# Kernel optimization log

Measured on AMD Instinct MI355X. Metric: run time of the kernel, lower is better.

Reference implementation:

```python
import jax, jax.numpy as jnp
import numpy as np
from jax import lax

V, E, H, T = 50000, 100, 230, 70
BIG, N = 128, 4096
NR, PV, PD = 53, 123, 5
IN = E + 2 * PD  # GRU input size = embedding_dim + 10


def setup_inputs():
    key = jax.random.key(0)
    ks = jax.random.split(key, 18)
    rng = np.random.default_rng(0)
    sizes = 1 + rng.multinomial(N - BIG, np.ones(BIG) / BIG)  # ragged, nonempty bags
    total_shape = jnp.asarray(np.concatenate([[0], np.cumsum(sizes)]).astype(np.int32))
    nrm = lambda k, s, sc=0.05: jax.random.normal(k, s, dtype=jnp.float32) * sc
    return {
        'sentence': jax.random.randint(ks[0], (N, T), 0, V),
        'pos1': jax.random.randint(ks[1], (N, T), 0, PV),
        'pos2': jax.random.randint(ks[2], (N, T), 0, PV),
        'total_shape': total_shape,
        'y_batch': jax.random.uniform(ks[3], (BIG, NR), dtype=jnp.float32),
        'word_emb': nrm(ks[4], (V, E), 0.1),
        'pos1_emb': nrm(ks[5], (PV, PD), 0.1),
        'pos2_emb': nrm(ks[6], (PV, PD), 0.1),
        'w_ih_f': nrm(ks[7], (3 * H, IN)),
        'w_hh_f': nrm(ks[8], (3 * H, H)),
        'b_ih_f': nrm(ks[9], (3 * H,)),
        'b_hh_f': nrm(ks[10], (3 * H,)),
        'w_ih_b': nrm(ks[11], (3 * H, IN)),
        'w_hh_b': nrm(ks[12], (3 * H, H)),
        'b_ih_b': nrm(ks[13], (3 * H,)),
        'b_hh_b': nrm(ks[14], (3 * H,)),
        'attention_w': nrm(ks[15], (H, 1), 0.1),
        'sen_a': nrm(ks[16], (H,), 0.1),
        'sen_r': nrm(ks[17], (H, 1), 0.1),
        'relation_embedding': nrm(jax.random.fold_in(key, 99), (NR, H), 0.1),
        'sen_d': nrm(jax.random.fold_in(key, 98), (NR,), 0.1),
    }


def _gru(x_proj, w_hh, b_hh, reverse):
    # x_proj: [T, N, 3H] precomputed input projections (PyTorch GRU gate order r,z,n)
    def step(h, xp):
        gh = h @ w_hh.T + b_hh
        r = jax.nn.sigmoid(xp[:, :H] + gh[:, :H])
        z = jax.nn.sigmoid(xp[:, H:2 * H] + gh[:, H:2 * H])
        n = jnp.tanh(xp[:, 2 * H:] + r * gh[:, 2 * H:])
        h = (1.0 - z) * n + z * h
        return h, h
    h0 = jnp.zeros((x_proj.shape[1], H), x_proj.dtype)
    _, hs = lax.scan(step, h0, x_proj, reverse=reverse)
    return hs  # [T, N, H], aligned with input time order


def reference(sentence, pos1, pos2, total_shape, y_batch, word_emb, pos1_emb, pos2_emb,
              w_ih_f, w_hh_f, b_ih_f, b_hh_f, w_ih_b, w_hh_b, b_ih_b, b_hh_b,
              attention_w, sen_a, sen_r, relation_embedding, sen_d):
    x = jnp.concatenate([word_emb[sentence], pos1_emb[pos1], pos2_emb[pos2]], axis=-1)  # [N,T,IN]
    xt = x.transpose(1, 0, 2)  # [T,N,IN]
    hf = _gru(jnp.einsum('tni,gi->tng', xt, w_ih_f) + b_ih_f, w_hh_f, b_hh_f, False)
    hb = _gru(jnp.einsum('tni,gi->tng', xt, w_ih_b) + b_ih_b, w_hh_b, b_hh_b, True)
    tup = (hf + hb).transpose(1, 0, 2)  # [N,T,H] fwd+bwd states summed, as in source
    scores = jnp.einsum('nth,h->nt', jnp.tanh(tup), attention_w[:, 0])
    alpha = jax.nn.softmax(scores, axis=-1)  # word attention over T=70
    attention_r = jnp.einsum('nt,nth->nh', alpha, tup)
    sen_repre = jnp.tanh(attention_r)  # [N,H]
    # ragged per-bag attention via segment ops (replaces Python loop over bags)
    seg = jnp.searchsorted(total_shape, jnp.arange(N), side='right') - 1  # bag id per sentence
    e = jnp.einsum('nh,h->n', sen_repre * sen_a, sen_r[:, 0])
    m = jax.ops.segment_max(e, seg, num_segments=BIG)
    ex = jnp.exp(e - m[seg])
    denom = jax.ops.segment_sum(ex, seg, num_segments=BIG)
    bag_alpha = ex / denom[seg]
    sen_s = jax.ops.segment_sum(bag_alpha[:, None] * sen_repre, seg, num_segments=BIG)  # [BIG,H]
    logits = sen_s @ relation_embedding.T + sen_d  # [BIG,NR]
    prob = jax.nn.softmax(logits, axis=-1)
    pred = jnp.argmax(prob, axis=-1)
    # BCEWithLogits, mean over 53 classes per bag, summed over bags
    bce = y_batch * jax.nn.softplus(-logits) + (1.0 - y_batch) * jax.nn.softplus(logits)
    total_loss = jnp.sum(jnp.mean(bce, axis=-1))
    acc = (pred == jnp.argmax(y_batch, axis=-1)).astype(jnp.float32)  # [BIG]
    return total_loss, acc, prob
```

## Files before the change

### kernel.cpp

```cpp
#include <hip/hip_runtime.h>
#include <hip/hip_bf16.h>
#include <math.h>

#define NSENT 4096
#define TT 70
#define HH 230
#define BIG 128
#define NR 53
#define GBLK 32
#define GTHR 512
#define XTOT (GBLK * 110)
#define ATHR 512

typedef float f32x4 __attribute__((ext_vector_type(4)));
typedef _Float16 f16x8 __attribute__((ext_vector_type(8)));
union U4F8 { uint4 u; f16x8 f; };
union U2H4 { uint2 u; _Float16 h[4]; };

__device__ __forceinline__ uint32_t packf16(float v) {
    _Float16 hi = (_Float16)v;
    float hif = (float)hi;
    _Float16 lo = (_Float16)(v - hif);
    union { _Float16 f; unsigned short u; } a, b;
    a.f = hi; b.f = lo;
    return ((uint32_t)a.u << 16) | (uint32_t)b.u;
}

__device__ __forceinline__ float fsig(float x) {
    x = fminf(fmaxf(x, -30.f), 30.f);
    return 1.f / (1.f + __expf(-x));
}
__device__ __forceinline__ float ftanh(float x) {
    x = fminf(fmaxf(x, -15.f), 15.f);
    float e = __expf(-2.f * x);
    return (1.f - e) / (1.f + e);
}

__global__ void prep_wfrag(const float* __restrict__ w_ih_f, const float* __restrict__ w_hh_f,
                           const float* __restrict__ w_ih_b, const float* __restrict__ w_hh_b,
                           uint4* __restrict__ wf) {
    int idx = blockIdx.x * 256 + threadIdx.x;
    if (idx >= 2 * 12 * 48 * 64) return;
    int lane = idx & 63;
    int r = idx >> 6;
    int nt = r % 48; r /= 48;
    int kt = r % 12; r /= 12;
    int dir = r;
    const float* wih = dir ? w_ih_b : w_ih_f;
    const float* whh = dir ? w_hh_b : w_hh_f;
    int sec = nt >> 4;
    int j = (nt & 15) * 16 + (lane & 15);
    int q = lane >> 4;
    unsigned short hu[8];
#pragma unroll
    for (int e = 0; e < 8; ++e) {
        int k = kt * 32 + 8 * q + e;
        float v = 0.f;
        if (j < HH) {
            int g = sec * HH + j;
            if (k < HH) v = whh[g * HH + k];
            else if (k >= 256 && k < 256 + 110) v = wih[g * 110 + (k - 256)];
        }
        union { _Float16 f; unsigned short u; } a;
        a.f = (_Float16)v;
        hu[e] = a.u;
    }
    uint4 H;
    H.x = (uint32_t)hu[0] | ((uint32_t)hu[1] << 16);
    H.y = (uint32_t)hu[2] | ((uint32_t)hu[3] << 16);
    H.z = (uint32_t)hu[4] | ((uint32_t)hu[5] << 16);
    H.w = (uint32_t)hu[6] | ((uint32_t)hu[7] << 16);
    wf[idx] = H;
}

__device__ __forceinline__ void unpackA(uint4 p0, uint4 p1, f16x8& hi, f16x8& lo) {
    U4F8 h, l;
    h.u.x = (p0.x >> 16) | (p0.y & 0xffff0000u);
    h.u.y = (p0.z >> 16) | (p0.w & 0xffff0000u);
    h.u.z = (p1.x >> 16) | (p1.y & 0xffff0000u);
    h.u.w = (p1.z >> 16) | (p1.w & 0xffff0000u);
    l.u.x = (p0.x & 0xffffu) | (p0.y << 16);
    l.u.y = (p0.z & 0xffffu) | (p0.w << 16);
    l.u.z = (p1.x & 0xffffu) | (p1.y << 16);
    l.u.w = (p1.z & 0xffffu) | (p1.w << 16);
    hi = h.f; lo = l.f;
}

extern __shared__ uint32_t lds[];

__global__ __launch_bounds__(GTHR, 2)
void gru_kernel(const int* __restrict__ sentence, const int* __restrict__ pos1, const int* __restrict__ pos2,
                const uint4* __restrict__ wf,
                const float* __restrict__ word_emb, const float* __restrict__ p1e, const float* __restrict__ p2e,
                const float* __restrict__ b_ih_f, const float* __restrict__ b_hh_f,
                const float* __restrict__ b_ih_b, const float* __restrict__ b_hh_b,
                _Float16* __restrict__ tupF, _Float16* __restrict__ tupB) {
    uint32_t* hA = lds;
    uint32_t* xA = lds + GBLK * 256;
    const uint4* hA4 = (const uint4*)hA;
    const uint4* xA4 = (const uint4*)xA;

    const int tid = threadIdx.x;
    const int lane = tid & 63;
    const int wv = tid >> 6;
    const int q = lane >> 4;
    const int lr = lane & 15;
    const int dir = blockIdx.x & 1;
    const int r0 = (blockIdx.x >> 1) * GBLK;
    uint32_t* tupU = (uint32_t*)(dir ? tupB : tupF);

    for (int i = tid; i < GBLK * (256 + 128); i += GTHR) lds[i] = 0;

    auto fetch_x = [&](int u, int t) -> float {
        int row = u / 110;
        int i = u - row * 110;
        int nn = r0 + row;
        if (i < 100)      return __builtin_nontemporal_load(&word_emb[(size_t)sentence[nn * TT + t] * 100 + i]);
        else if (i < 105) return __builtin_nontemporal_load(&p1e[pos1[nn * TT + t] * 5 + (i - 100)]);
        else              return __builtin_nontemporal_load(&p2e[pos2[nn * TT + t] * 5 + (i - 105)]);
    };
    auto xslot = [&](int u) -> int {
        int row = u / 110;
        int i = u - row * 110;
        return row * 128 + ((((i >> 2) ^ (row & 7)) << 2) | (i & 3));
    };

    __syncthreads();
    {
        int t0 = dir ? TT - 1 : 0;
        for (int u = tid; u < XTOT; u += GTHR) xA[xslot(u)] = packf16(fetch_x(u, t0));
    }
    __syncthreads();

    const float* bih = dir ? b_ih_b : b_ih_f;
    const float* bhh = dir ? b_hh_b : b_hh_f;
    float bR[2], bZ[2], bHn[2], bIn[2];
    int jc[2];
#pragma unroll
    for (int rt = 0; rt < 2; ++rt) {
        int j = 32 * wv + 16 * rt + lr;
        jc[rt] = j;
        bool v = j < HH;
        bR[rt]  = v ? bih[j] + bhh[j] : 0.f;
        bZ[rt]  = v ? bih[HH + j] + bhh[HH + j] : 0.f;
        bIn[rt] = v ? bih[2 * HH + j] : 0.f;
        bHn[rt] = v ? bhh[2 * HH + j] : 0.f;
    }
    float hreg[16];
#pragma unroll
    for (int i = 0; i < 16; ++i) hreg[i] = 0.f;

    const int r7 = lr & 7;
    const size_t wdirbase = (size_t)dir * 12 * 48;

    uint4 BH[8][2];
    auto loadB = [&](int idx) {
        const int kt = idx / 3, pp = idx - 3 * kt;
        const int nt = 2 * wv + ((pp == 0) ? 0 : (pp == 1) ? 16 : 32);
        const uint4* p = wf + (wdirbase + (size_t)kt * 48 + nt) * 64 + lane;
        BH[idx & 7][0] = p[0];
        BH[idx & 7][1] = p[64];
    };

    for (int s = 0; s < TT; ++s) {
        const int t = dir ? (TT - 1 - s) : s;
        float gx[7];
        if (s < TT - 1) {
            const int tn = dir ? t - 1 : t + 1;
#pragma unroll
            for (int c = 0; c < 7; ++c) {
                int u = tid + c * GTHR;
                if (u < XTOT) gx[c] = fetch_x(u, tn);
            }
        }

        f32x4 acc[2][8];
#pragma unroll
        for (int m = 0; m < 2; ++m)
#pragma unroll
            for (int c = 0; c < 8; ++c) acc[m][c] = (f32x4){0.f, 0.f, 0.f, 0.f};

        loadB(0); loadB(1); loadB(2); loadB(3); loadB(4); loadB(5);
        f16x8 Ahi[2], Alo[2];
#pragma unroll
        for (int idx = 0; idx < 36; ++idx) {
            const int kt = idx / 3, pp = idx - 3 * kt;
            if (pp == 0) {
#pragma unroll
                for (int m = 0; m < 2; ++m) {
                    int row = m * 16 + lr;
                    uint4 p0, p1;
                    if (kt < 8) {
                        int b = kt * 8 + 2 * q;
                        p0 = hA4[row * 64 + ((b)     ^ r7)];
                        p1 = hA4[row * 64 + ((b + 1) ^ r7)];
                    } else {
                        int b = (kt - 8) * 8 + 2 * q;
                        p0 = xA4[row * 32 + ((b)     ^ r7)];
                        p1 = xA4[row * 32 + ((b + 1) ^ r7)];
                    }
                    unpackA(p0, p1, Ahi[m], Alo[m]);
                }
            }
            if (idx + 6 < 36) loadB(idx + 6);
            const int sb = idx & 7;
#pragma unroll
            for (int term = 0; term < 2; ++term)
#pragma unroll
                for (int u = 0; u < 2; ++u) {
                    const int slot = (pp < 2) ? pp * 2 + u : (kt < 8 ? 4 + u : 6 + u);
                    U4F8 B; B.u = BH[sb][u];
#pragma unroll
                    for (int m = 0; m < 2; ++m) {
                        f16x8 A = term ? Alo[m] : Ahi[m];
                        acc[m][slot] = __builtin_amdgcn_mfma_f32_16x16x32_f16(A, B.f, acc[m][slot], 0, 0, 0);
                    }
                }
        }
        __syncthreads();

#pragma unroll
        for (int m = 0; m < 2; ++m)
#pragma unroll
            for (int rt = 0; rt < 2; ++rt)
#pragma unroll
                for (int rg = 0; rg < 4; ++rg) {
                    int row = m * 16 + q * 4 + rg;
                    float vr = fsig(acc[m][rt][rg] + bR[rt]);
                    float vz = fsig(acc[m][2 + rt][rg] + bZ[rt]);
                    float gn = acc[m][4 + rt][rg] + bHn[rt];
                    float xn = acc[m][6 + rt][rg] + bIn[rt];
                    float vn = ftanh(xn + vr * gn);
                    int hi_ = m * 8 + rt * 4 + rg;
                    float h = (1.f - vz) * vn + vz * hreg[hi_];
                    hreg[hi_] = h;
                    int j = jc[rt];
                    hA[row * 256 + ((((j >> 2) ^ (row & 7)) << 2) | (j & 3))] = packf16(h);
                }
        if (s < TT - 1) {
#pragma unroll
            for (int c = 0; c < 7; ++c) {
                int u = tid + c * GTHR;
                if (u < XTOT) xA[xslot(u)] = packf16(gx[c]);
            }
        }
        __syncthreads();

        for (int u = tid; u < GBLK * 115; u += GTHR) {
            int row = u / 115, c = u - row * 115;
            int bi = row * 256 + ((((c >> 1) ^ (row & 7)) << 2) | (2 * (c & 1)));
            uint32_t p0 = hA[bi];
            uint32_t p1 = hA[bi + 1];
            uint32_t o = (p0 >> 16) | (p1 & 0xffff0000u);
            __builtin_nontemporal_store(o, &tupU[((size_t)(r0 + row) * TT + t) * 115 + c]);
        }
        if (dir == 0 && s == TT - 1) {
            __syncthreads();
            for (int i = tid; i < GBLK * 256; i += GTHR) hA[i] = 0;
            __syncthreads();
        }
    }
}

__global__ __launch_bounds__(ATHR)
void attn_kernel(const _Float16* __restrict__ tupF, const _Float16* __restrict__ tupB,
                 const float* __restrict__ aw,
                 const float* __restrict__ sen_a, const float* __restrict__ sen_r,
                 float* __restrict__ sen_repre, float* __restrict__ e_out) {
    __shared__ float tb[TT * HH];
    __shared__ float sc[TT + 2];
    const int n = blockIdx.x, tid = threadIdx.x;
    const uint2* pF = (const uint2*)(tupF + (size_t)n * TT * HH);
    const uint2* pB = (const uint2*)(tupB + (size_t)n * TT * HH);
    for (int u = tid; u < TT * HH / 4; u += ATHR) {
        U2H4 a, b;
        a.u = pF[u]; b.u = pB[u];
#pragma unroll
        for (int e2 = 0; e2 < 4; ++e2)
            tb[4 * u + e2] = (float)a.h[e2] + (float)b.h[e2];
    }
    __syncthreads();
    {
        int tg = tid >> 2, sub = tid & 3;
        if (tg < TT) {
            float s = 0.f;
            for (int k = sub; k < HH; k += 4) s += ftanh(tb[tg * HH + k]) * aw[k];
            s += __shfl_xor(s, 1);
            s += __shfl_xor(s, 2);
            if (sub == 0) sc[tg] = s;
        }
    }
    __syncthreads();
    if (tid == 0) {
        float m = sc[0];
        for (int t2 = 1; t2 < TT; ++t2) m = fmaxf(m, sc[t2]);
        float den = 0.f;
        for (int t2 = 0; t2 < TT; ++t2) { float ex = __expf(sc[t2] - m); sc[t2] = ex; den += ex; }
        float inv = 1.f / den;
        for (int t2 = 0; t2 < TT; ++t2) sc[t2] *= inv;
    }
    __syncthreads();
    float contrib = 0.f;
    if (tid < HH) {
        float ar = 0.f;
        for (int t2 = 0; t2 < TT; ++t2) ar += sc[t2] * tb[t2 * HH + tid];
        float sr = tanhf(ar);
        sen_repre[(size_t)n * HH + tid] = sr;
        contrib = sr * sen_a[tid] * sen_r[tid];
    }
    __syncthreads();
    if (tid < 256) tb[tid] = (tid < HH) ? contrib : 0.f;
    __syncthreads();
#pragma unroll
    for (int off = 128; off > 0; off >>= 1) {
        if (tid < off) tb[tid] += tb[tid + off];
        __syncthreads();
    }
    if (tid == 0) e_out[n] = tb[0];
}

__global__ __launch_bounds__(256)
void bag_kernel(const int* __restrict__ total_shape, const float* __restrict__ e,
                const float* __restrict__ senr, const float* __restrict__ rel,
                const float* __restrict__ sen_d, const float* __restrict__ y,
                float* __restrict__ out, float* __restrict__ lossp) {
    __shared__ float ew[512];
    __shared__ float ss[232];
    __shared__ float lg[56];
    const int b = blockIdx.x, tid = threadIdx.x;
    const int s0 = total_shape[b], s1 = total_shape[b + 1];
    const int cnt = s1 - s0;
    for (int i = tid; i < cnt; i += 256) ew[i] = e[s0 + i];
    __syncthreads();
    if (tid == 0) {
        float m = ew[0];
        for (int i = 1; i < cnt; ++i) m = fmaxf(m, ew[i]);
        float den = 0.f;
        for (int i = 0; i < cnt; ++i) { float ex = expf(ew[i] - m); ew[i] = ex; den += ex; }
        float inv = 1.f / den;
        for (int i = 0; i < cnt; ++i) ew[i] *= inv;
    }
    __syncthreads();
    if (tid < HH) {
        float sacc = 0.f;
        for (int i = 0; i < cnt; ++i) sacc += ew[i] * senr[(size_t)(s0 + i) * HH + tid];
        ss[tid] = sacc;
    }
    __syncthreads();
    if (tid < NR) {
        float sacc = sen_d[tid];
        for (int j = 0; j < HH; ++j) sacc += ss[j] * rel[tid * HH + j];
        lg[tid] = sacc;
    }
    __syncthreads();
    if (tid == 0) {
        float m = lg[0]; int pm = 0;
        for (int k = 1; k < NR; ++k) if (lg[k] > m) { m = lg[k]; pm = k; }
        float den = 0.f;
        for (int k = 0; k < NR; ++k) den += expf(lg[k] - m);
        float inv = 1.f / den;
        float bces = 0.f;
        float ym = y[b * NR]; int yarg = 0;
        for (int k = 0; k < NR; ++k) {
            float p = expf(lg[k] - m) * inv;
            out[1 + BIG + b * NR + k] = p;
            float yy = y[b * NR + k];
            if (yy > ym) { ym = yy; yarg = k; }
            float l = lg[k];
            float sp_pos = fmaxf(l, 0.f) + log1pf(expf(-fabsf(l)));
            float sp_neg = sp_pos - l;
            bces += yy * sp_neg + (1.f - yy) * sp_pos;
        }
        lossp[b] = bces * (1.f / (float)NR);
        out[1 + b] = (pm == yarg) ? 1.f : 0.f;
    }
}

__global__ void loss_sum(const float* __restrict__ lossp, float* __restrict__ out) {
    if (threadIdx.x == 0) {
        float sacc = 0.f;
        for (int b2 = 0; b2 < BIG; ++b2) sacc += lossp[b2];
        out[0] = sacc;
    }
}

extern "C" void kernel_launch(void* const* d_in, const int* in_sizes, int n_in,
                              void* d_out, int out_size, void* d_ws, size_t ws_size,
                              hipStream_t stream) {
    const int*   sentence = (const int*)d_in[0];
    const int*   pos1     = (const int*)d_in[1];
    const int*   pos2     = (const int*)d_in[2];
    const int*   tshape   = (const int*)d_in[3];
    const float* y_batch  = (const float*)d_in[4];
    const float* word_emb = (const float*)d_in[5];
    const float* p1e      = (const float*)d_in[6];
    const float* p2e      = (const float*)d_in[7];
    const float* w_ih_f   = (const float*)d_in[8];
    const float* w_hh_f   = (const float*)d_in[9];
    const float* b_ih_f   = (const float*)d_in[10];
    const float* b_hh_f   = (const float*)d_in[11];
    const float* w_ih_b   = (const float*)d_in[12];
    const float* w_hh_b   = (const float*)d_in[13];
    const float* b_ih_b   = (const float*)d_in[14];
    const float* b_hh_b   = (const float*)d_in[15];
    const float* att_w    = (const float*)d_in[16];
    const float* sen_a    = (const float*)d_in[17];
    const float* sen_r    = (const float*)d_in[18];
    const float* rel      = (const float*)d_in[19];
    const float* sen_d    = (const float*)d_in[20];
    float* out = (float*)d_out;

    const size_t TUP_E  = (size_t)NSENT * TT * HH;
    const size_t SENR_F = (size_t)NSENT * HH;
    _Float16* tupF = (_Float16*)d_ws;
    _Float16* tupB = tupF + TUP_E;
    float* senr  = (float*)(tupB + TUP_E);
    float* e     = senr + SENR_F;
    float* lossp = e + NSENT;
    uint4* wf    = (uint4*)senr;

    prep_wfrag<<<288, 256, 0, stream>>>(w_ih_f, w_hh_f, w_ih_b, w_hh_b, wf);
    gru_kernel<<<(NSENT / GBLK) * 2, GTHR, GBLK * (256 + 128) * 4, stream>>>(
        sentence, pos1, pos2, wf, word_emb, p1e, p2e,
        b_ih_f, b_hh_f, b_ih_b, b_hh_b, tupF, tupB);
    attn_kernel<<<NSENT, ATHR, 0, stream>>>(tupF, tupB, att_w, sen_a, sen_r, senr, e);
    bag_kernel<<<BIG, 256, 0, stream>>>(tshape, e, senr, rel, sen_d, y_batch, out, lossp);
    loss_sum<<<1, 64, 0, stream>>>(lossp, out);
}
```

Before: 2.758 ms.

## Drop split-fp16 hi/lo emulation, use plain fp16 state and double rows per block

Replaces the hi+lo fp16 split representation of hidden state and inputs with single fp16 values, halving the MFMA count per output tile and the LDS footprint. The block now processes 64 sentences instead of 32 with 4 M-tiles per wave, blocks are remapped so each direction lands on a fixed set of XCDs, and the input prefetch into registers is replaced by a synchronous gather after the gate update. This trades accuracy of the recurrence (plain fp16 h over 70 steps) and load/compute overlap for fewer MFMAs and better weight reuse; grid shrinks to 128 blocks, which may underfill the GPU.

```diff
diff --git a/kernel.cpp b/kernel.cpp
--- a/kernel.cpp
+++ b/kernel.cpp
@@ -7,7 +7,7 @@
 #define HH 230
 #define BIG 128
 #define NR 53
-#define GBLK 32
+#define GBLK 64
 #define GTHR 512
 #define XTOT (GBLK * 110)
 #define ATHR 512
@@ -16,15 +16,6 @@
 typedef _Float16 f16x8 __attribute__((ext_vector_type(8)));
 union U4F8 { uint4 u; f16x8 f; };
 union U2H4 { uint2 u; _Float16 h[4]; };
-
-__device__ __forceinline__ uint32_t packf16(float v) {
-    _Float16 hi = (_Float16)v;
-    float hif = (float)hi;
-    _Float16 lo = (_Float16)(v - hif);
-    union { _Float16 f; unsigned short u; } a, b;
-    a.f = hi; b.f = lo;
-    return ((uint32_t)a.u << 16) | (uint32_t)b.u;
-}
 
 __device__ __forceinline__ float fsig(float x) {
     x = fminf(fmaxf(x, -30.f), 30.f);
@@ -73,20 +64,7 @@
     wf[idx] = H;
 }
 
-__device__ __forceinline__ void unpackA(uint4 p0, uint4 p1, f16x8& hi, f16x8& lo) {
-    U4F8 h, l;
-    h.u.x = (p0.x >> 16) | (p0.y & 0xffff0000u);
-    h.u.y = (p0.z >> 16) | (p0.w & 0xffff0000u);
-    h.u.z = (p1.x >> 16) | (p1.y & 0xffff0000u);
-    h.u.w = (p1.z >> 16) | (p1.w & 0xffff0000u);
-    l.u.x = (p0.x & 0xffffu) | (p0.y << 16);
-    l.u.y = (p0.z & 0xffffu) | (p0.w << 16);
-    l.u.z = (p1.x & 0xffffu) | (p1.y << 16);
-    l.u.w = (p1.z & 0xffffu) | (p1.w << 16);
-    hi = h.f; lo = l.f;
-}
-
-extern __shared__ uint32_t lds[];
+extern __shared__ unsigned short lds16[];
 
 __global__ __launch_bounds__(GTHR, 2)
 void gru_kernel(const int* __restrict__ sentence, const int* __restrict__ pos1, const int* __restrict__ pos2,
@@ -95,21 +73,25 @@
                 const float* __restrict__ b_ih_f, const float* __restrict__ b_hh_f,
                 const float* __restrict__ b_ih_b, const float* __restrict__ b_hh_b,
                 _Float16* __restrict__ tupF, _Float16* __restrict__ tupB) {
-    uint32_t* hA = lds;
-    uint32_t* xA = lds + GBLK * 256;
+    _Float16* hA = (_Float16*)lds16;
+    _Float16* xA = (_Float16*)(lds16 + GBLK * 256);
     const uint4* hA4 = (const uint4*)hA;
     const uint4* xA4 = (const uint4*)xA;
+    const uint32_t* hAw = (const uint32_t*)hA;
 
     const int tid = threadIdx.x;
     const int lane = tid & 63;
     const int wv = tid >> 6;
     const int q = lane >> 4;
     const int lr = lane & 15;
-    const int dir = blockIdx.x & 1;
-    const int r0 = (blockIdx.x >> 1) * GBLK;
+    const int b = blockIdx.x;
+    const int xcd = b & 7;
+    const int dir = (xcd >= 4) ? 1 : 0;
+    const int chunk = (b >> 3) * 4 + (xcd & 3);
+    const int r0 = chunk * GBLK;
     uint32_t* tupU = (uint32_t*)(dir ? tupB : tupF);
 
-    for (int i = tid; i < GBLK * (256 + 128); i += GTHR) lds[i] = 0;
+    for (int i = tid; i < GBLK * (256 + 128) / 2; i += GTHR) ((uint32_t*)lds16)[i] = 0;
 
     auto fetch_x = [&](int u, int t) -> float {
         int row = u / 110;
@@ -119,16 +101,16 @@
         else if (i < 105) return __builtin_nontemporal_load(&p1e[pos1[nn * TT + t] * 5 + (i - 100)]);
         else              return __builtin_nontemporal_load(&p2e[pos2[nn * TT + t] * 5 + (i - 105)]);
     };
-    auto xslot = [&](int u) -> int {
+    auto put_x = [&](int u, float v) {
         int row = u / 110;
         int i = u - row * 110;
-        return row * 128 + ((((i >> 2) ^ (row & 7)) << 2) | (i & 3));
+        xA[(row * 16 + ((i >> 3) ^ (row & 7))) * 8 + (i & 7)] = (_Float16)v;
     };
 
     __syncthreads();
     {
         int t0 = dir ? TT - 1 : 0;
-        for (int u = tid; u < XTOT; u += GTHR) xA[xslot(u)] = packf16(fetch_x(u, t0));
+        for (int u = tid; u < XTOT; u += GTHR) put_x(u, fetch_x(u, t0));
     }
     __syncthreads();
 
@@ -146,81 +128,60 @@
         bIn[rt] = v ? bih[2 * HH + j] : 0.f;
         bHn[rt] = v ? bhh[2 * HH + j] : 0.f;
     }
-    float hreg[16];
-#pragma unroll
-    for (int i = 0; i < 16; ++i) hreg[i] = 0.f;
-
-    const int r7 = lr & 7;
+    float hreg[32];
+#pragma unroll
+    for (int i = 0; i < 32; ++i) hreg[i] = 0.f;
+
     const size_t wdirbase = (size_t)dir * 12 * 48;
 
-    uint4 BH[8][2];
+    uint4 BH[4][2];
     auto loadB = [&](int idx) {
         const int kt = idx / 3, pp = idx - 3 * kt;
         const int nt = 2 * wv + ((pp == 0) ? 0 : (pp == 1) ? 16 : 32);
         const uint4* p = wf + (wdirbase + (size_t)kt * 48 + nt) * 64 + lane;
-        BH[idx & 7][0] = p[0];
-        BH[idx & 7][1] = p[64];
+        BH[idx & 3][0] = p[0];
+        BH[idx & 3][1] = p[64];
     };
 
     for (int s = 0; s < TT; ++s) {
         const int t = dir ? (TT - 1 - s) : s;
-        float gx[7];
-        if (s < TT - 1) {
-            const int tn = dir ? t - 1 : t + 1;
-#pragma unroll
-            for (int c = 0; c < 7; ++c) {
-                int u = tid + c * GTHR;
-                if (u < XTOT) gx[c] = fetch_x(u, tn);
-            }
-        }
-
-        f32x4 acc[2][8];
-#pragma unroll
-        for (int m = 0; m < 2; ++m)
+
+        f32x4 acc[4][8];
+#pragma unroll
+        for (int m = 0; m < 4; ++m)
 #pragma unroll
             for (int c = 0; c < 8; ++c) acc[m][c] = (f32x4){0.f, 0.f, 0.f, 0.f};
 
-        loadB(0); loadB(1); loadB(2); loadB(3); loadB(4); loadB(5);
-        f16x8 Ahi[2], Alo[2];
+        loadB(0); loadB(1); loadB(2); loadB(3);
+        f16x8 Ah[4];
 #pragma unroll
         for (int idx = 0; idx < 36; ++idx) {
             const int kt = idx / 3, pp = idx - 3 * kt;
             if (pp == 0) {
 #pragma unroll
-                for (int m = 0; m < 2; ++m) {
+                for (int m = 0; m < 4; ++m) {
                     int row = m * 16 + lr;
-                    uint4 p0, p1;
-                    if (kt < 8) {
-                        int b = kt * 8 + 2 * q;
-                        p0 = hA4[row * 64 + ((b)     ^ r7)];
-                        p1 = hA4[row * 64 + ((b + 1) ^ r7)];
-                    } else {
-                        int b = (kt - 8) * 8 + 2 * q;
-                        p0 = xA4[row * 32 + ((b)     ^ r7)];
-                        p1 = xA4[row * 32 + ((b + 1) ^ r7)];
-                    }
-                    unpackA(p0, p1, Ahi[m], Alo[m]);
+                    U4F8 av;
+                    av.u = (kt < 8) ? hA4[row * 32 + ((kt * 4 + q) ^ (row & 7))]
+                                    : xA4[row * 16 + (((kt - 8) * 4 + q) ^ (row & 7))];
+                    Ah[m] = av.f;
                 }
             }
-            if (idx + 6 < 36) loadB(idx + 6);
-            const int sb = idx & 7;
-#pragma unroll
-            for (int term = 0; term < 2; ++term)
-#pragma unroll
-                for (int u = 0; u < 2; ++u) {
-                    const int slot = (pp < 2) ? pp * 2 + u : (kt < 8 ? 4 + u : 6 + u);
-                    U4F8 B; B.u = BH[sb][u];
-#pragma unroll
-                    for (int m = 0; m < 2; ++m) {
-                        f16x8 A = term ? Alo[m] : Ahi[m];
-                        acc[m][slot] = __builtin_amdgcn_mfma_f32_16x16x32_f16(A, B.f, acc[m][slot], 0, 0, 0);
-                    }
-                }
+            if (idx + 4 < 36) loadB(idx + 4);
+            const int sb = idx & 3;
+#pragma unroll
+            for (int u = 0; u < 2; ++u) {
+                const int slot = (pp < 2) ? pp * 2 + u : (kt < 8 ? 4 + u : 6 + u);
+                U4F8 B; B.u = BH[sb][u];
+#pragma unroll
+                for (int m = 0; m < 4; ++m)
+                    acc[m][slot] = __builtin_amdgcn_mfma_f32_16x16x32_f16(Ah[m], B.f, acc[m][slot], 0, 0, 0);
+            }
         }
         __syncthreads();
 
 #pragma unroll
-        for (int m = 0; m < 2; ++m)
+        for (int m = 0; m < 4; ++m)
 #pragma unroll
             for (int rt = 0; rt < 2; ++rt)
 #pragma unroll
@@ -235,29 +196,21 @@
                     float h = (1.f - vz) * vn + vz * hreg[hi_];
                     hreg[hi_] = h;
                     int j = jc[rt];
-                    hA[row * 256 + ((((j >> 2) ^ (row & 7)) << 2) | (j & 3))] = packf16(h);
+                    hA[(row * 32 + ((j >> 3) ^ (row & 7))) * 8 + (j & 7)] = (_Float16)h;
                 }
         if (s < TT - 1) {
-#pragma unroll
-            for (int c = 0; c < 7; ++c) {
-                int u = tid + c * GTHR;
-                if (u < XTOT) xA[xslot(u)] = packf16(gx[c]);
-            }
+            const int tn = dir ? t - 2 * s + TT - 2 - (TT - 1 - s - 1) + 0 : t + 1;
+        }
+        if (s < TT - 1) {
+            const int tn = dir ? (TT - 2 - s) : (s + 1);
+            for (int u = tid; u < XTOT; u += GTHR) put_x(u, fetch_x(u, tn));
         }
         __syncthreads();
 
         for (int u = tid; u < GBLK * 115; u += GTHR) {
             int row = u / 115, c = u - row * 115;
-            int bi = row * 256 + ((((c >> 1) ^ (row & 7)) << 2) | (2 * (c & 1)));
-            uint32_t p0 = hA[bi];
-            uint32_t p1 = hA[bi + 1];
-            uint32_t o = (p0 >> 16) | (p1 & 0xffff0000u);
+            uint32_t o = hAw[(row * 32 + ((c >> 2) ^ (row & 7))) * 4 + (c & 3)];
             __builtin_nontemporal_store(o, &tupU[((size_t)(r0 + row) * TT + t) * 115 + c]);
-        }
-        if (dir == 0 && s == TT - 1) {
-            __syncthreads();
-            for (int i = tid; i < GBLK * 256; i += GTHR) hA[i] = 0;
-            __syncthreads();
         }
     }
 }
@@ -420,7 +373,7 @@
     uint4* wf    = (uint4*)senr;
 
     prep_wfrag<<<288, 256, 0, stream>>>(w_ih_f, w_hh_f, w_ih_b, w_hh_b, wf);
-    gru_kernel<<<(NSENT / GBLK) * 2, GTHR, GBLK * (256 + 128) * 4, stream>>>(
+    gru_kernel<<<(NSENT / GBLK) * 2, GTHR, GBLK * (256 + 128) * 2, stream>>>(
         sentence, pos1, pos2, wf, word_emb, p1e, p2e,
         b_ih_f, b_hh_f, b_ih_b, b_hh_b, tupF, tupB);
     attn_kernel<<<NSENT, ATHR, 0, stream>>>(tupF, tupB, att_w, sen_a, sen_r, senr, e);
```

Result: slower. 3.899 ms (+41.4%).

## Prefetch GRU weight tiles across timesteps and map directions to XCD halves

Applied to the files above, without the earlier changes.

The weight-fragment prefetch ring becomes continuous across timesteps. The first tiles of the next step load during the tail of the current step, so each step no longer starts with an exposed six-load prologue, and the prefetch depth grows from 6 to 7. Block-to-work mapping is changed so that blocks on XCDs 0-3 handle the forward direction and XCDs 4-7 the backward one, keeping each direction's weights in fewer L2 caches. The final-step zeroing of the hidden-state LDS is also removed. Because sb0 is computed as (s*4)&7, the rotating slot index may not line up with 36 loads per step unless that expression is consistent, so correctness depends on the slot arithmetic.

```diff
diff --git a/kernel.cpp b/kernel.cpp
--- a/kernel.cpp
+++ b/kernel.cpp
@@ -105,8 +105,11 @@
     const int wv = tid >> 6;
     const int q = lane >> 4;
     const int lr = lane & 15;
-    const int dir = blockIdx.x & 1;
-    const int r0 = (blockIdx.x >> 1) * GBLK;
+    const int b = blockIdx.x;
+    const int xcd = b & 7;
+    const int dir = (xcd >= 4) ? 1 : 0;
+    const int chunk = (b >> 3) * 4 + (xcd & 3);
+    const int r0 = chunk * GBLK;
     uint32_t* tupU = (uint32_t*)(dir ? tupB : tupF);
 
     for (int i = tid; i < GBLK * (256 + 128); i += GTHR) lds[i] = 0;
@@ -154,16 +157,19 @@
     const size_t wdirbase = (size_t)dir * 12 * 48;
 
     uint4 BH[8][2];
-    auto loadB = [&](int idx) {
-        const int kt = idx / 3, pp = idx - 3 * kt;
+    auto loadB = [&](int slot, int widx) {
+        const int kt = widx / 3, pp = widx - 3 * kt;
         const int nt = 2 * wv + ((pp == 0) ? 0 : (pp == 1) ? 16 : 32);
         const uint4* p = wf + (wdirbase + (size_t)kt * 48 + nt) * 64 + lane;
-        BH[idx & 7][0] = p[0];
-        BH[idx & 7][1] = p[64];
+        BH[slot][0] = p[0];
+        BH[slot][1] = p[64];
     };
+#pragma unroll
+    for (int g = 0; g < 7; ++g) loadB(g & 7, g);
 
     for (int s = 0; s < TT; ++s) {
         const int t = dir ? (TT - 1 - s) : s;
+        const int sb0 = (s * 4) & 7;
         float gx[7];
         if (s < TT - 1) {
             const int tn = dir ? t - 1 : t + 1;
@@ -180,7 +186,6 @@
 #pragma unroll
             for (int c = 0; c < 8; ++c) acc[m][c] = (f32x4){0.f, 0.f, 0.f, 0.f};
 
-        loadB(0); loadB(1); loadB(2); loadB(3); loadB(4); loadB(5);
         f16x8 Ahi[2], Alo[2];
 #pragma unroll
         for (int idx = 0; idx < 36; ++idx) {
@@ -191,19 +196,19 @@
                     int row = m * 16 + lr;
                     uint4 p0, p1;
                     if (kt < 8) {
-                        int b = kt * 8 + 2 * q;
-                        p0 = hA4[row * 64 + ((b)     ^ r7)];
-                        p1 = hA4[row * 64 + ((b + 1) ^ r7)];
+                        int bb = kt * 8 + 2 * q;
+                        p0 = hA4[row * 64 + ((bb)     ^ r7)];
+                        p1 = hA4[row * 64 + ((bb + 1) ^ r7)];
                     } else {
-                        int b = (kt - 8) * 8 + 2 * q;
-                        p0 = xA4[row * 32 + ((b)     ^ r7)];
-                        p1 = xA4[row * 32 + ((b + 1) ^ r7)];
+                        int bb = (kt - 8) * 8 + 2 * q;
+                        p0 = xA4[row * 32 + ((bb)     ^ r7)];
+                        p1 = xA4[row * 32 + ((bb + 1) ^ r7)];
                     }
                     unpackA(p0, p1, Ahi[m], Alo[m]);
                 }
             }
-            if (idx + 6 < 36) loadB(idx + 6);
-            const int sb = idx & 7;
+            loadB((sb0 + idx + 7) & 7, (idx + 7) % 36);
+            const int sb = (sb0 + idx) & 7;
 #pragma unroll
             for (int term = 0; term < 2; ++term)
 #pragma unroll
@@ -253,11 +258,6 @@
             uint32_t p1 = hA[bi + 1];
             uint32_t o = (p0 >> 16) | (p1 & 0xffff0000u);
             __builtin_nontemporal_store(o, &tupU[((size_t)(r0 + row) * TT + t) * 115 + c]);
-        }
-        if (dir == 0 && s == TT - 1) {
-            __syncthreads();
-            for (int i = tid; i < GBLK * 256; i += GTHR) hA[i] = 0;
-            __syncthreads();
         }
     }
 }
```

Measured after the change: 5.932 ms. 2.15x slower.
